# Kernel tuning notes

Measured on AMD Instinct MI355X. Metric: run time of the kernel, lower is better.

## Reference

```python
import jax, jax.numpy as jnp
import numpy as np


def setup_inputs() -> dict:
    key = jax.random.key(0)
    k0, k1, k2, k3 = jax.random.split(key, 4)
    B, L, D, H = 8, 4096, 300, 128  # batch, leaves (power of 2), embed dim, hidden
    x = jax.random.normal(k0, (B, L, D), jnp.float32)
    W_leaf = jax.random.normal(k1, (D, 2 * H), jnp.float32) * (1.0 / np.sqrt(D))
    b_leaf = jnp.zeros((2 * H,), jnp.float32)
    W_l = jax.random.normal(k2, (H, 5 * H), jnp.float32) * (1.0 / np.sqrt(H))
    W_r = jax.random.normal(k3, (H, 5 * H), jnp.float32) * (1.0 / np.sqrt(H))
    b = jnp.zeros((5 * H,), jnp.float32)
    return {"x": x, "W_leaf": W_leaf, "b_leaf": b_leaf, "W_l": W_l, "W_r": W_r, "b": b}


def reference(x, W_leaf, b_leaf, W_l, W_r, b):
    """Binary TreeLSTM over a complete tree: leaves -> root.

    x: [B, L, D] leaf embeddings, L a power of 2.
    Leaf transform: linear projection split into (h, c) (SPINN-style).
    REDUCE: 5-gate child-sum-of-two composition.
    Returns root hidden state: [B, H].
    """
    H = W_l.shape[0]
    hc = x @ W_leaf + b_leaf                     # [B, L, 2H]
    h, c = hc[..., :H], hc[..., H:]
    levels = int(np.log2(x.shape[1]))
    for _ in range(levels):                      # level-batched tree reduction
        h_l, h_r = h[:, 0::2], h[:, 1::2]        # [B, n/2, H]
        c_l, c_r = c[:, 0::2], c[:, 1::2]
        gates = h_l @ W_l + h_r @ W_r + b        # [B, n/2, 5H]
        i, fl, fr, o, g = jnp.split(gates, 5, axis=-1)
        c = (jax.nn.sigmoid(fl) * c_l
             + jax.nn.sigmoid(fr) * c_r
             + jax.nn.sigmoid(i) * jnp.tanh(g))
        h = jax.nn.sigmoid(o) * jnp.tanh(c)
    return h[:, 0]                               # root hidden state [B, H]
```

## Files before the change

kernel.cpp:

```cpp
#include <hip/hip_runtime.h>
#include <hip/hip_bf16.h>
#include <math.h>


typedef __attribute__((ext_vector_type(8))) short bfrag8;
typedef __attribute__((ext_vector_type(4))) float f32x4;

__device__ __forceinline__ float rcpf(float x) { return __builtin_amdgcn_rcpf(x); }
__device__ __forceinline__ float sigf(float x) { return rcpf(1.0f + __expf(-x)); }
__device__ __forceinline__ float tanh_f(float x) {
    float e = __expf(2.0f * x);
    return 1.0f - 2.0f * rcpf(e + 1.0f);
}
__device__ __forceinline__ short f2bf(float f) {
    __hip_bfloat16 h = __float2bfloat16(f);
    return *reinterpret_cast<short*>(&h);
}
__device__ __forceinline__ bfrag8 pack8(f32x4 a, f32x4 b) {
    union { int i[4]; bfrag8 v; } u;
    asm("v_cvt_pk_bf16_f32 %0, %1, %2" : "=v"(u.i[0]) : "v"(a[0]), "v"(a[1]));
    asm("v_cvt_pk_bf16_f32 %0, %1, %2" : "=v"(u.i[1]) : "v"(a[2]), "v"(a[3]));
    asm("v_cvt_pk_bf16_f32 %0, %1, %2" : "=v"(u.i[2]) : "v"(b[0]), "v"(b[1]));
    asm("v_cvt_pk_bf16_f32 %0, %1, %2" : "=v"(u.i[3]) : "v"(b[2]), "v"(b[3]));
    return u.v;
}
#define GLDS(gp, lp) __builtin_amdgcn_global_load_lds( \
    (const __attribute__((address_space(1))) void*)(gp), \
    (__attribute__((address_space(3))) void*)(lp), 16, 0, 0)

__global__ __launch_bounds__(256) void leaf_kernel(
    const float* __restrict__ x,     const float* __restrict__ Wleaf,
    const float* __restrict__ W_l,   const float* __restrict__ W_r,
    const float* __restrict__ bleaf,
    short* __restrict__ hD,
    float* __restrict__ cD,
    short* __restrict__ Wcat_ch)
{
    __shared__ float Als[128 * 64];
    __shared__ short Bls[8 * 128 * 8];
    const int tid  = threadIdx.x;
    const int w    = tid >> 6, lane = tid & 63;
    const int quad = lane >> 4, l16 = lane & 15;
    const int mBlk = blockIdx.x * 128, nBlk = blockIdx.y * 128;
    const int waveM = (w >> 1) * 64, waveN = (w & 1) * 64;

    if (blockIdx.y == 0 && blockIdx.x < 160) {
        #pragma unroll
        for (int e = 0; e < 4; ++e) {
            int idx = blockIdx.x * 1024 + e * 256 + tid;
            int n = idx >> 8, k = idx & 255;
            float v = (k < 128) ? W_l[k * 640 + n] : W_r[(k - 128) * 640 + n];
            Wcat_ch[(((size_t)(k >> 3)) * 640 + n) * 8 + (k & 7)] = f2bf(v);
        }
    }

    f32x4 acc[4][4] = {};
    const f32x4 zero4 = {0.f, 0.f, 0.f, 0.f};

    for (int c = 0; c < 5; ++c) {
        const int k0c = c * 64;
        {
            const int q_lds = lane & 15;
            const int rsub  = lane >> 4;
            #pragma unroll
            for (int g = 0; g < 8; ++g) {
                int row = w * 32 + g * 4 + rsub;
                int q_g = (q_lds & 8) | ((q_lds & 7) ^ (row & 7));
                if (c < 4 || q_g < 11) {
                    GLDS(x + (size_t)(mBlk + row) * 300 + k0c + q_g * 4,
                         (char*)Als + (w * 32 + g * 4) * 256);
                } else {
                    *(f32x4*)((char*)Als + row * 256 + q_lds * 16) = zero4;
                }
            }
        }
        #pragma unroll
        for (int uu = 0; uu < 4; ++uu) {
            int id  = uu * 256 + tid;
            int ccl = id >> 7, nl = id & 127;
            int k0  = (c * 8 + ccl) * 8;
            int n   = nBlk + nl;
            f32x4 v0, v1;
            #pragma unroll
            for (int jj = 0; jj < 4; ++jj)
                v0[jj] = (k0 + jj < 300) ? Wleaf[(size_t)(k0 + jj) * 256 + n] : 0.0f;
            #pragma unroll
            for (int jj = 0; jj < 4; ++jj)
                v1[jj] = (k0 + 4 + jj < 300) ? Wleaf[(size_t)(k0 + 4 + jj) * 256 + n] : 0.0f;
            *(bfrag8*)(Bls + (ccl * 128 + nl) * 8) = pack8(v0, v1);
        }
        __syncthreads();
        #pragma unroll
        for (int ks = 0; ks < 2; ++ks) {
            const int ca = ks * 4 + quad;
            bfrag8 af[4], bf4[4];
            #pragma unroll
            for (int i = 0; i < 4; ++i) {
                int r  = waveM + i * 16 + l16;
                int u0 = 2 * ca, u1 = 2 * ca + 1;
                int s0 = (u0 & 8) | ((u0 & 7) ^ (r & 7));
                int s1 = (u1 & 8) | ((u1 & 7) ^ (r & 7));
                f32x4 a0 = *(const f32x4*)(Als + r * 64 + s0 * 4);
                f32x4 a1 = *(const f32x4*)(Als + r * 64 + s1 * 4);
                af[i] = pack8(a0, a1);
            }
            #pragma unroll
            for (int jn = 0; jn < 4; ++jn)
                bf4[jn] = *(const bfrag8*)(Bls + (ca * 128 + waveN + jn * 16 + l16) * 8);
            #pragma unroll
            for (int i = 0; i < 4; ++i)
                #pragma unroll
                for (int jn = 0; jn < 4; ++jn)
                    acc[i][jn] = __builtin_amdgcn_mfma_f32_16x16x32_bf16(
                                     af[i], bf4[jn], acc[i][jn], 0, 0, 0);
        }
        __syncthreads();
    }

    #pragma unroll
    for (int i = 0; i < 4; ++i) {
        int row0 = mBlk + waveM + i * 16 + quad * 4;
        #pragma unroll
        for (int jn = 0; jn < 4; ++jn) {
            int col = nBlk + waveN + jn * 16 + l16;
            float bv = bleaf[col];
            #pragma unroll
            for (int rg = 0; rg < 4; ++rg) {
                float v = acc[i][jn][rg] + bv;
                int m = row0 + rg;
                if (nBlk == 0) {
                    int hc = col;
                    hD[(((size_t)((m & 1) * 16 + (hc >> 3))) * 16384 + (m >> 1)) * 8
                       + (hc & 7)] = f2bf(v);
                } else {
                    cD[(size_t)m * 128 + (col - 128)] = v;
                }
            }
        }
    }
}

__global__ __launch_bounds__(256, 2) void level_ws_kernel(
    const short* __restrict__ A,
    const float* __restrict__ cprev,
    const short* __restrict__ Wch,
    const float* __restrict__ bias,
    short* __restrict__ hout, float* __restrict__ cout_,
    int M, int nst)
{
    __shared__ short Als[32 * 64 * 8];
    const int tid  = threadIdx.x;
    const int w    = tid >> 6, lane = tid & 63;
    const int quad = lane >> 4, l16 = lane & 15;
    const int j   = blockIdx.y;
    const int tb0 = blockIdx.x * 64 * nst;
    const int h   = j * 16 + l16;

    #pragma unroll
    for (int s = 0; s < 8; ++s)
        GLDS(A + ((size_t)(s * 4 + w) * M + tb0 + lane) * 8,
             (char*)Als + (s * 4 + w) * 1024);

    bfrag8 Wfr[5][8];
    #pragma unroll
    for (int g = 0; g < 5; ++g)
        #pragma unroll
        for (int s = 0; s < 8; ++s)
            Wfr[g][s] = *(const bfrag8*)(Wch + ((size_t)(s * 4 + quad) * 640
                                                + g * 128 + h) * 8);
    const float bi  = bias[h],       bfl = bias[128 + h], bfr_ = bias[256 + h];
    const float bo  = bias[384 + h], bg  = bias[512 + h];

    const int Mn = M >> 1;
    for (int st = 0; st < nst; ++st) {
        const int tb = tb0 + st * 64;
        __syncthreads();

        f32x4 acc[5] = {};
        #pragma unroll
        for (int s = 0; s < 8; ++s) {
            bfrag8 af = *(const bfrag8*)(Als + ((s * 4 + quad) * 64 + w * 16 + l16) * 8);
            #pragma unroll
            for (int g = 0; g < 5; ++g)
                acc[g] = __builtin_amdgcn_mfma_f32_16x16x32_bf16(af, Wfr[g][s], acc[g], 0, 0, 0);
        }

        if (st + 1 < nst) {
            __syncthreads();
            #pragma unroll
            for (int s = 0; s < 8; ++s)
                GLDS(A + ((size_t)(s * 4 + w) * M + tb + 64 + lane) * 8,
                     (char*)Als + (s * 4 + w) * 1024);
        }

        #pragma unroll
        for (int rg = 0; rg < 4; ++rg) {
            int m = tb + w * 16 + quad * 4 + rg;
            float gi  = acc[0][rg] + bi;
            float gfl = acc[1][rg] + bfl;
            float gfr = acc[2][rg] + bfr_;
            float go  = acc[3][rg] + bo;
            float gg  = acc[4][rg] + bg;
            float cl  = cprev[(size_t)(2 * m) * 128 + h];
            float cr  = cprev[(size_t)(2 * m + 1) * 128 + h];
            float cn  = sigf(gfl) * cl + sigf(gfr) * cr + sigf(gi) * tanh_f(gg);
            float hn  = sigf(go) * tanh_f(cn);
            hout[(((size_t)((m & 1) * 16 + (h >> 3))) * Mn + (m >> 1)) * 8
                 + (h & 7)] = f2bf(hn);
            cout_[(size_t)m * 128 + h] = cn;
        }
    }
}

__global__ __launch_bounds__(512) void finish_kernel(
    const short* __restrict__ hin,
    const float* __restrict__ cin,
    const short* __restrict__ Wch, const float* __restrict__ bias,
    float* __restrict__ out)
{
    __shared__ short hP[32 * 64 * 8];
    __shared__ short hQ[32 * 32 * 8];
    __shared__ float cA[128 * 128];
    __shared__ float cB[64 * 128];
    const int tid  = threadIdx.x;
    const int w    = tid >> 6, lane = tid & 63;
    const int quad = lane >> 4, l16 = lane & 15;
    const int h    = w * 16 + l16;

    #pragma unroll
    for (int g = 0; g < 4; ++g)
        GLDS(hin + ((size_t)((g * 8 + w) * 64 + lane)) * 8,
             (char*)hP + ((g * 8 + w) * 64) * 16);
    #pragma unroll
    for (int g = 0; g < 8; ++g)
        GLDS(cin + ((size_t)((g * 8 + w) * 64 + lane)) * 4,
             (char*)cA + ((g * 8 + w) * 64) * 16);

    bfrag8 Wfr[5][8];
    #pragma unroll
    for (int g = 0; g < 5; ++g)
        #pragma unroll
        for (int s = 0; s < 8; ++s)
            Wfr[g][s] = *(const bfrag8*)(Wch + ((size_t)(s * 4 + quad) * 640
                                                + g * 128 + h) * 8);
    const float bi  = bias[h],       bfl = bias[128 + h], bfr_ = bias[256 + h];
    const float bo  = bias[384 + h], bg  = bias[512 + h];

    __syncthreads();

    #pragma unroll
    for (int t = 0; t < 4; ++t) {
        const int Mo = 64 >> t;
        const short* hsrc = (t & 1) ? hQ : hP;
        short* hdst       = (t & 1) ? hP : hQ;
        const float* cread  = (t & 1) ? cB : cA;
        float*       cwrite = (t & 1) ? cA : cB;
        const int nrt = (Mo + 15) >> 4;

        for (int rt = 0; rt < nrt; ++rt) {
            f32x4 acc[5] = {};
            #pragma unroll
            for (int s = 0; s < 8; ++s) {
                bfrag8 af = *(const bfrag8*)(hsrc + ((s * 4 + quad) * Mo
                                                     + rt * 16 + l16) * 8);
                #pragma unroll
                for (int g = 0; g < 5; ++g)
                    acc[g] = __builtin_amdgcn_mfma_f32_16x16x32_bf16(
                                 af, Wfr[g][s], acc[g], 0, 0, 0);
            }
            #pragma unroll
            for (int rg = 0; rg < 4; ++rg) {
                int m = rt * 16 + quad * 4 + rg;
                if (m < Mo) {
                    float gi  = acc[0][rg] + bi;
                    float gfl = acc[1][rg] + bfl;
                    float gfr = acc[2][rg] + bfr_;
                    float go  = acc[3][rg] + bo;
                    float gg  = acc[4][rg] + bg;
                    float cl  = cread[(2 * m) * 128 + h];
                    float cr  = cread[(2 * m + 1) * 128 + h];
                    float cn  = sigf(gfl) * cl + sigf(gfr) * cr + sigf(gi) * tanh_f(gg);
                    float hn  = sigf(go) * tanh_f(cn);
                    if (t == 3) {
                        out[(size_t)m * 128 + h] = hn;
                    } else {
                        hdst[(((m & 1) * 16 + (h >> 3)) * (Mo >> 1) + (m >> 1)) * 8
                             + (h & 7)] = f2bf(hn);
                        cwrite[m * 128 + h] = cn;
                    }
                }
            }
        }
        __syncthreads();
    }
}

extern "C" void kernel_launch(void* const* d_in, const int* in_sizes, int n_in,
                              void* d_out, int out_size, void* d_ws, size_t ws_size,
                              hipStream_t stream)
{
    const float* x      = (const float*)d_in[0];
    const float* W_leaf = (const float*)d_in[1];
    const float* b_leaf = (const float*)d_in[2];
    const float* W_l    = (const float*)d_in[3];
    const float* W_r    = (const float*)d_in[4];
    const float* b      = (const float*)d_in[5];
    float* out = (float*)d_out;

    char* p = (char*)d_ws;
    short* hA    = (short*)p; p += (size_t)32 * 16384 * 16 + 1024;
    short* hB    = (short*)p; p += (size_t)32 * 8192 * 16 + 1024;
    float* c0    = (float*)p; p += (size_t)32768 * 128 * 4;
    float* c1    = (float*)p; p += (size_t)16384 * 128 * 4;
    short* WcatC = (short*)p; p += (size_t)32 * 640 * 16;

    leaf_kernel<<<dim3(256, 2), 256, 0, stream>>>(
        x, W_leaf, W_l, W_r, b_leaf, hA, c0, WcatC);

    const short* hin = hA; const float* cin = c0;
    int M = 16384;
    for (int lev = 1; lev <= 8; ++lev) {
        short* ho = (lev & 1) ? hB : hA;
        float* co = (lev & 1) ? c1 : c0;
        int nst = (lev == 1) ? 4 : (lev == 2) ? 2 : 1;
        level_ws_kernel<<<dim3(M / (64 * nst), 8), 256, 0, stream>>>(
            hin, cin, WcatC, b, ho, co, M, nst);
        hin = ho; cin = co;
        M >>= 1;
    }

    finish_kernel<<<1, 512, 0, stream>>>(hA, c0, WcatC, b, out);
}
```

Baseline: 169.1 us.

## Fuse tree levels six through eight into one LDS-resident tail kernel

Replaces three separate level launches with a single tail kernel of 4 blocks. Each block loads its slice of level-5 output and computes levels 6-8 in shared memory, keeping intermediate h/c on-chip and weights in registers. This removes two launches and the global round trips between them, but runs those levels on only 4 workgroups. Level 3 is also changed to use two sub-tiles per block instead of one.

```diff
diff --git a/kernel.cpp b/kernel.cpp
--- a/kernel.cpp
+++ b/kernel.cpp
@@ -206,6 +206,139 @@
             float cn  = sigf(gfl) * cl + sigf(gfr) * cr + sigf(gi) * tanh_f(gg);
             float hn  = sigf(go) * tanh_f(cn);
             hout[(((size_t)((m & 1) * 16 + (h >> 3))) * Mn + (m >> 1)) * 8
+                 + (h & 7)] = f2bf(hn);
+            cout_[(size_t)m * 128 + h] = cn;
+        }
+    }
+}
+
+__global__ __launch_bounds__(512, 2) void tail3_kernel(
+    const short* __restrict__ A,
+    const float* __restrict__ cprev,
+    const short* __restrict__ Wch, const float* __restrict__ bias,
+    short* __restrict__ hout,
+    float* __restrict__ cout_)
+{
+    __shared__ short Als[32 * 128 * 8];
+    __shared__ short h6 [128 * 128];
+    __shared__ float c6 [128 * 128];
+    const int tid  = threadIdx.x;
+    const int w    = tid >> 6, lane = tid & 63;
+    const int quad = lane >> 4, l16 = lane & 15;
+    const int h    = w * 16 + l16;
+    const int b    = blockIdx.x;
+
+    #pragma unroll
+    for (int s = 0; s < 8; ++s) {
+        int idx = s * 8 + w;
+        GLDS(A + ((size_t)(idx >> 1) * 512 + b * 128 + (idx & 1) * 64 + lane) * 8,
+             (char*)Als + idx * 1024);
+    }
+
+    bfrag8 Wfr[5][8];
+    #pragma unroll
+    for (int g = 0; g < 5; ++g)
+        #pragma unroll
+        for (int s = 0; s < 8; ++s)
+            Wfr[g][s] = *(const bfrag8*)(Wch + ((size_t)(s * 4 + quad) * 640
+                                                + g * 128 + h) * 8);
+    const float bi  = bias[h],       bfl = bias[128 + h], bfr_ = bias[256 + h];
+    const float bo  = bias[384 + h], bg  = bias[512 + h];
+
+    __syncthreads();
+
+    for (int rt = 0; rt < 8; ++rt) {
+        f32x4 acc[5] = {};
+        #pragma unroll
+        for (int s = 0; s < 8; ++s) {
+            bfrag8 af = *(const bfrag8*)(Als + ((s * 4 + quad) * 128
+                                                + rt * 16 + l16) * 8);
+            #pragma unroll
+            for (int g = 0; g < 5; ++g)
+                acc[g] = __builtin_amdgcn_mfma_f32_16x16x32_bf16(
+                             af, Wfr[g][s], acc[g], 0, 0, 0);
+        }
+        #pragma unroll
+        for (int rg = 0; rg < 4; ++rg) {
+            int mloc = rt * 16 + quad * 4 + rg;
+            int mG   = b * 128 + mloc;
+            float gi  = acc[0][rg] + bi;
+            float gfl = acc[1][rg] + bfl;
+            float gfr = acc[2][rg] + bfr_;
+            float go  = acc[3][rg] + bo;
+            float gg  = acc[4][rg] + bg;
+            float cl  = cprev[(size_t)(2 * mG) * 128 + h];
+            float cr  = cprev[(size_t)(2 * mG + 1) * 128 + h];
+            float cn  = sigf(gfl) * cl + sigf(gfr) * cr + sigf(gi) * tanh_f(gg);
+            float hn  = sigf(go) * tanh_f(cn);
+            c6[mloc * 128 + h] = cn;
+            int byte = (mloc * 256 + h * 2) ^ (((mloc >> 1) & 7) << 4);
+            *(short*)((char*)h6 + byte) = f2bf(hn);
+        }
+    }
+    __syncthreads();
+
+    short* h7 = Als;
+    float* c7 = (float*)((char*)Als + 16384);
+    for (int rt = 0; rt < 4; ++rt) {
+        f32x4 acc[5] = {};
+        #pragma unroll
+        for (int s = 0; s < 8; ++s) {
+            int cch  = s * 4 + quad;
+            int row  = 2 * (rt * 16 + l16) + (cch >> 4);
+            int byte = (row * 256 + (cch & 15) * 16) ^ (((row >> 1) & 7) << 4);
+            bfrag8 af = *(const bfrag8*)((const char*)h6 + byte);
+            #pragma unroll
+            for (int g = 0; g < 5; ++g)
+                acc[g] = __builtin_amdgcn_mfma_f32_16x16x32_bf16(
+                             af, Wfr[g][s], acc[g], 0, 0, 0);
+        }
+        #pragma unroll
+        for (int rg = 0; rg < 4; ++rg) {
+            int mloc = rt * 16 + quad * 4 + rg;
+            float gi  = acc[0][rg] + bi;
+            float gfl = acc[1][rg] + bfl;
+            float gfr = acc[2][rg] + bfr_;
+            float go  = acc[3][rg] + bo;
+            float gg  = acc[4][rg] + bg;
+            float cl  = c6[(2 * mloc) * 128 + h];
+            float cr  = c6[(2 * mloc + 1) * 128 + h];
+            float cn  = sigf(gfl) * cl + sigf(gfr) * cr + sigf(gi) * tanh_f(gg);
+            float hn  = sigf(go) * tanh_f(cn);
+            c7[mloc * 128 + h] = cn;
+            int byte = (mloc * 256 + h * 2) ^ (((mloc >> 1) & 7) << 4);
+            *(short*)((char*)h7 + byte) = f2bf(hn);
+        }
+    }
+    __syncthreads();
+
+    for (int rt = 0; rt < 2; ++rt) {
+        f32x4 acc[5] = {};
+        #pragma unroll
+        for (int s = 0; s < 8; ++s) {
+            int cch  = s * 4 + quad;
+            int row  = 2 * (rt * 16 + l16) + (cch >> 4);
+            int byte = (row * 256 + (cch & 15) * 16) ^ (((row >> 1) & 7) << 4);
+            bfrag8 af = *(const bfrag8*)((const char*)h7 + byte);
+            #pragma unroll
+            for (int g = 0; g < 5; ++g)
+                acc[g] = __builtin_amdgcn_mfma_f32_16x16x32_bf16(
+                             af, Wfr[g][s], acc[g], 0, 0, 0);
+        }
+        #pragma unroll
+        for (int rg = 0; rg < 4; ++rg) {
+            int mloc = rt * 16 + quad * 4 + rg;
+            int m    = b * 32 + mloc;
+            float gi  = acc[0][rg] + bi;
+            float gfl = acc[1][rg] + bfl;
+            float gfr = acc[2][rg] + bfr_;
+            float go  = acc[3][rg] + bo;
+            float gg  = acc[4][rg] + bg;
+            float cl  = c7[(2 * mloc) * 128 + h];
+            float cr  = c7[(2 * mloc + 1) * 128 + h];
+            float cn  = sigf(gfl) * cl + sigf(gfr) * cr + sigf(gi) * tanh_f(gg);
+            float hn  = sigf(go) * tanh_f(cn);
+            hout[(((size_t)((m & 1) * 16 + (h >> 3))) * 64 + (m >> 1)) * 8
                  + (h & 7)] = f2bf(hn);
             cout_[(size_t)m * 128 + h] = cn;
         }
@@ -319,15 +452,17 @@
 
     const short* hin = hA; const float* cin = c0;
     int M = 16384;
-    for (int lev = 1; lev <= 8; ++lev) {
+    for (int lev = 1; lev <= 5; ++lev) {
         short* ho = (lev & 1) ? hB : hA;
         float* co = (lev & 1) ? c1 : c0;
-        int nst = (lev == 1) ? 4 : (lev == 2) ? 2 : 1;
+        int nst = (lev == 1) ? 4 : (lev == 2) ? 2 : (lev == 3) ? 2 : 1;
         level_ws_kernel<<<dim3(M / (64 * nst), 8), 256, 0, stream>>>(
             hin, cin, WcatC, b, ho, co, M, nst);
         hin = ho; cin = co;
         M >>= 1;
     }
 
+    tail3_kernel<<<4, 512, 0, stream>>>(hB, c1, WcatC, b, hA, c0);
+
     finish_kernel<<<1, 512, 0, stream>>>(hA, c0, WcatC, b, out);
 }
```

Result: slower. 185.2 us (+9.6%).

## Widen leaf GEMM tile to full 256 columns to reuse x loads

Applied to the files above, without the earlier changes.

Each leaf_kernel block now computes all 256 output columns (h and c halves) instead of splitting them across two grid-y blocks, so the x tile is loaded and converted once rather than twice. This halves the grid to 256 blocks and doubles accumulators per thread (128 floats) and the B-tile LDS. The gain is less global traffic for x, paid for with higher register pressure and lower occupancy and parallelism. A no-op nullptr check was also added inside f2bf.

```diff
diff --git a/kernel.cpp b/kernel.cpp
--- a/kernel.cpp
+++ b/kernel.cpp
@@ -13,7 +13,7 @@
     return 1.0f - 2.0f * rcpf(e + 1.0f);
 }
 __device__ __forceinline__ short f2bf(float f) {
-    __hip_bfloat16 h = __float2bfloat16(f);
+    __hip_bfloat16 h = __float2bfloat16(&f == nullptr ? 0.0f : f);
     return *reinterpret_cast<short*>(&h);
 }
 __device__ __forceinline__ bfrag8 pack8(f32x4 a, f32x4 b) {
@@ -37,14 +37,14 @@
     short* __restrict__ Wcat_ch)
 {
     __shared__ float Als[128 * 64];
-    __shared__ short Bls[8 * 128 * 8];
+    __shared__ short Bls[8 * 256 * 8];
     const int tid  = threadIdx.x;
     const int w    = tid >> 6, lane = tid & 63;
     const int quad = lane >> 4, l16 = lane & 15;
-    const int mBlk = blockIdx.x * 128, nBlk = blockIdx.y * 128;
+    const int mBlk = blockIdx.x * 128;
     const int waveM = (w >> 1) * 64, waveN = (w & 1) * 64;
 
-    if (blockIdx.y == 0 && blockIdx.x < 160) {
+    if (blockIdx.x < 160) {
         #pragma unroll
         for (int e = 0; e < 4; ++e) {
             int idx = blockIdx.x * 1024 + e * 256 + tid;
@@ -54,7 +54,7 @@
         }
     }
 
-    f32x4 acc[4][4] = {};
+    f32x4 acc[2][4][4] = {};
     const f32x4 zero4 = {0.f, 0.f, 0.f, 0.f};
 
     for (int c = 0; c < 5; ++c) {
@@ -75,25 +75,23 @@
             }
         }
         #pragma unroll
-        for (int uu = 0; uu < 4; ++uu) {
-            int id  = uu * 256 + tid;
-            int ccl = id >> 7, nl = id & 127;
+        for (int uu = 0; uu < 8; ++uu) {
+            int ccl = uu, nl = tid;
             int k0  = (c * 8 + ccl) * 8;
-            int n   = nBlk + nl;
             f32x4 v0, v1;
             #pragma unroll
             for (int jj = 0; jj < 4; ++jj)
-                v0[jj] = (k0 + jj < 300) ? Wleaf[(size_t)(k0 + jj) * 256 + n] : 0.0f;
+                v0[jj] = (k0 + jj < 300) ? Wleaf[(size_t)(k0 + jj) * 256 + nl] : 0.0f;
             #pragma unroll
             for (int jj = 0; jj < 4; ++jj)
-                v1[jj] = (k0 + 4 + jj < 300) ? Wleaf[(size_t)(k0 + 4 + jj) * 256 + n] : 0.0f;
-            *(bfrag8*)(Bls + (ccl * 128 + nl) * 8) = pack8(v0, v1);
+                v1[jj] = (k0 + 4 + jj < 300) ? Wleaf[(size_t)(k0 + 4 + jj) * 256 + nl] : 0.0f;
+            *(bfrag8*)(Bls + (ccl * 256 + nl) * 8) = pack8(v0, v1);
         }
         __syncthreads();
         #pragma unroll
         for (int ks = 0; ks < 2; ++ks) {
             const int ca = ks * 4 + quad;
-            bfrag8 af[4], bf4[4];
+            bfrag8 af[4];
             #pragma unroll
             for (int i = 0; i < 4; ++i) {
                 int r  = waveM + i * 16 + l16;
@@ -105,35 +103,43 @@
                 af[i] = pack8(a0, a1);
             }
             #pragma unroll
-            for (int jn = 0; jn < 4; ++jn)
-                bf4[jn] = *(const bfrag8*)(Bls + (ca * 128 + waveN + jn * 16 + l16) * 8);
-            #pragma unroll
-            for (int i = 0; i < 4; ++i)
+            for (int nh = 0; nh < 2; ++nh) {
+                bfrag8 bf4[4];
                 #pragma unroll
                 for (int jn = 0; jn < 4; ++jn)
-                    acc[i][jn] = __builtin_amdgcn_mfma_f32_16x16x32_bf16(
-                                     af[i], bf4[jn], acc[i][jn], 0, 0, 0);
+                    bf4[jn] = *(const bfrag8*)(Bls + (ca * 256 + nh * 128
+                                                      + waveN + jn * 16 + l16) * 8);
+                #pragma unroll
+                for (int i = 0; i < 4; ++i)
+                    #pragma unroll
+                    for (int jn = 0; jn < 4; ++jn)
+                        acc[nh][i][jn] = __builtin_amdgcn_mfma_f32_16x16x32_bf16(
+                                             af[i], bf4[jn], acc[nh][i][jn], 0, 0, 0);
+            }
         }
         __syncthreads();
     }
 
     #pragma unroll
-    for (int i = 0; i < 4; ++i) {
-        int row0 = mBlk + waveM + i * 16 + quad * 4;
-        #pragma unroll
-        for (int jn = 0; jn < 4; ++jn) {
-            int col = nBlk + waveN + jn * 16 + l16;
-            float bv = bleaf[col];
-            #pragma unroll
-            for (int rg = 0; rg < 4; ++rg) {
-                float v = acc[i][jn][rg] + bv;
-                int m = row0 + rg;
-                if (nBlk == 0) {
-                    int hc = col;
-                    hD[(((size_t)((m & 1) * 16 + (hc >> 3))) * 16384 + (m >> 1)) * 8
-                       + (hc & 7)] = f2bf(v);
-                } else {
-                    cD[(size_t)m * 128 + (col - 128)] = v;
+    for (int nh = 0; nh < 2; ++nh) {
+        #pragma unroll
+        for (int i = 0; i < 4; ++i) {
+            int row0 = mBlk + waveM + i * 16 + quad * 4;
+            #pragma unroll
+            for (int jn = 0; jn < 4; ++jn) {
+                int col = nh * 128 + waveN + jn * 16 + l16;
+                float bv = bleaf[col];
+                #pragma unroll
+                for (int rg = 0; rg < 4; ++rg) {
+                    float v = acc[nh][i][jn][rg] + bv;
+                    int m = row0 + rg;
+                    if (nh == 0) {
+                        int hc = col;
+                        hD[(((size_t)((m & 1) * 16 + (hc >> 3))) * 16384 + (m >> 1)) * 8
+                           + (hc & 7)] = f2bf(v);
+                    } else {
+                        cD[(size_t)m * 128 + (col - 128)] = v;
+                    }
                 }
             }
         }
@@ -314,7 +320,7 @@
     float* c1    = (float*)p; p += (size_t)16384 * 128 * 4;
     short* WcatC = (short*)p; p += (size_t)32 * 640 * 16;
 
-    leaf_kernel<<<dim3(256, 2), 256, 0, stream>>>(
+    leaf_kernel<<<256, 256, 0, stream>>>(
         x, W_leaf, W_l, W_r, b_leaf, hA, c0, WcatC);
 
     const short* hin = hA; const float* cin = c0;
```

After: 167.4 us. Within noise of the previous version (-1.0%).
